# Kernel optimization log

Hardware: AMD Instinct MI355X
Metric: run time of the kernel (lower is better)

The kernel has to match this reference:

```python
import jax, jax.numpy as jnp
import numpy as np

DIM, HEADS, DIM_HEAD = 512, 8, 64

def setup_inputs() -> dict:
    key = jax.random.key(0)
    ks = jax.random.split(key, 9)
    B, T = 4, 4096
    s = 1.0 / np.sqrt(DIM)
    x = jax.random.normal(ks[0], (B, T, DIM), dtype=jnp.float32)
    Wq = jax.random.uniform(ks[1], (DIM, DIM), jnp.float32, -s, s)
    Wk = jax.random.uniform(ks[2], (DIM, DIM), jnp.float32, -s, s)
    Wv = jax.random.uniform(ks[3], (DIM, DIM), jnp.float32, -s, s)
    Wp = jax.random.uniform(ks[4], (DIM, DIM), jnp.float32, -s, s)
    bq = jax.random.uniform(ks[5], (DIM,), jnp.float32, -s, s)
    bk = jax.random.uniform(ks[6], (DIM,), jnp.float32, -s, s)
    bv = jax.random.uniform(ks[7], (DIM,), jnp.float32, -s, s)
    bp = jax.random.uniform(ks[8], (DIM,), jnp.float32, -s, s)
    return {"x": x, "Wq": Wq, "bq": bq, "Wk": Wk, "bk": bk,
            "Wv": Wv, "bv": bv, "Wp": Wp, "bp": bp}

def reference(x, Wq, bq, Wk, bk, Wv, bv, Wp, bp):
    B, T, _ = x.shape
    H, D = HEADS, DIM_HEAD
    # projections -> [B, H, T, D]
    def proj(W, b):
        return (x @ W.T + b).reshape(B, T, H, D).transpose(0, 2, 1, 3)
    q = jax.nn.softmax(proj(Wq, bq), axis=-1)
    k = jax.nn.softmax(proj(Wk, bk), axis=-1)
    v = proj(Wv, bv)
    # l1 normalization: D_inv = 1 / <q, sum_t k>
    k_sum = k.sum(axis=2, keepdims=True)                 # [B,H,1,D]
    D_inv = 1.0 / (q * k_sum).sum(axis=-1, keepdims=True)  # [B,H,T,1]
    context = jnp.einsum('bhtd,bhte->bhde', k, v)        # small DxD per head
    out = jnp.einsum('bhtd,bhde->bhte', q, context) * D_inv + q
    out = out.transpose(0, 2, 1, 3).reshape(B, T, H * D)
    return out @ Wp.T + bp
```

## Files before the change

kernel.cpp:

```cpp
#include <hip/hip_runtime.h>

#define NTOK  16384
#define KDIM  512
#define NQKV  1536
#define TT    4096

using frag8   = __attribute__((ext_vector_type(8))) short;
using floatx4 = __attribute__((ext_vector_type(4))) float;

__device__ __forceinline__ unsigned short f2b(float f) {
  union { float f; unsigned u; } v; v.f = f;
  unsigned r = v.u + 0x7fffu + ((v.u >> 16) & 1u);
  return (unsigned short)(r >> 16);
}
__device__ __forceinline__ float b2f(unsigned short s) {
  union { unsigned u; float f; } v; v.u = ((unsigned)s) << 16; return v.f;
}
__device__ __forceinline__ float blo(unsigned w) {
  union { unsigned u; float f; } v; v.u = w << 16; return v.f;
}
__device__ __forceinline__ float bhi(unsigned w) {
  union { unsigned u; float f; } v; v.u = w & 0xffff0000u; return v.f;
}

__device__ __forceinline__ void gl_lds16(const void* g, void* l) {
  __builtin_amdgcn_global_load_lds((__attribute__((address_space(1))) const void*)g,
                                   (__attribute__((address_space(3))) void*)l,
                                   16, 0, 0);
}

__global__ __launch_bounds__(256) void cvt_all(
    const float* __restrict__ x,
    const float* __restrict__ Wq, const float* __restrict__ Wk,
    const float* __restrict__ Wv, const float* __restrict__ Wp,
    const float* __restrict__ bq, const float* __restrict__ bk,
    const float* __restrict__ bv,
    unsigned short* __restrict__ xb,
    unsigned short* __restrict__ wqkv, unsigned short* __restrict__ wp,
    float* __restrict__ bias_qkv) {
  const int blk = blockIdx.x;
  if (blk < 8192) {
    const size_t i = (size_t)blk * 256 + threadIdx.x;
    const float4 v = ((const float4*)x)[i];
    ushort4 o;
    o.x = f2b(v.x); o.y = f2b(v.y); o.z = f2b(v.z); o.w = f2b(v.w);
    ((ushort4*)xb)[i] = o;
    return;
  }
  const int idx = (blk - 8192) * 256 + threadIdx.x;
  if (idx < 786432) {
    const int m = idx >> 9, i = idx & 511;
    const float* W = (m < 512) ? Wq : ((m < 1024) ? Wk : Wv);
    wqkv[idx] = f2b(W[(m & 511) * 512 + i]);
    return;
  }
  const int j = idx - 786432;
  if (j < 262144) { wp[j] = f2b(Wp[j]); return; }
  const int c = j - 262144;
  if (c < 1536)
    bias_qkv[c] = (c < 512) ? bq[c] : ((c < 1024) ? bk[c - 512] : bv[c - 1024]);
}

template<int SOFT>
__global__ __launch_bounds__(256, 2) void gemm_bt(
    const unsigned short* __restrict__ A,
    const unsigned short* __restrict__ Bm,
    const float* __restrict__ bias,
    void* __restrict__ C,
    int M, int N, int K, int ldc)
{
  __shared__ unsigned short sh[32768];
  const int tid  = threadIdx.x;
  const int wave = tid >> 6;
  const int lane = tid & 63;
  const int quad = lane >> 4;
  const int lr   = lane & 15;
  const int sw7  = lr & 7;
  const int bid  = ((blockIdx.x & 7) * (gridDim.x >> 3)) + (blockIdx.x >> 3);
  const int nt   = N >> 7;
  const int bn   = (bid % nt) << 7;
  const int bm   = (bid / nt) << 7;
  const int half = wave >> 1;
  const int wm   = half << 6;
  const int wn   = (wave & 1) << 6;

  floatx4 acc[4][4] = {};

  const int srow = tid >> 3;
  const int scol = ((tid & 7) ^ ((tid >> 3) & 7)) << 3;
  const unsigned short* Ag = A + (size_t)(bm + srow) * K + scol;
  const unsigned short* Bg = Bm + (size_t)(bn + srow) * K + scol;

  auto STAGE = [&](unsigned short* base, int k0) {
    unsigned short* Al = base + (wave << 9);
    unsigned short* Bl = Al + 8192;
    gl_lds16(Ag + k0,                    Al);
    gl_lds16(Ag + (size_t)32 * K + k0,   Al + 2048);
    gl_lds16(Ag + (size_t)64 * K + k0,   Al + 4096);
    gl_lds16(Ag + (size_t)96 * K + k0,   Al + 6144);
    gl_lds16(Bg + k0,                    Bl);
    gl_lds16(Bg + (size_t)32 * K + k0,   Bl + 2048);
    gl_lds16(Bg + (size_t)64 * K + k0,   Bl + 4096);
    gl_lds16(Bg + (size_t)96 * K + k0,   Bl + 6144);
  };

  auto COMPUTE = [&](const unsigned short* Asb) {
    const unsigned short* Bsb = Asb + 8192;
#pragma unroll
    for (int kk = 0; kk < 2; kk++) {
      const int coff = ((((kk << 2) + quad) ^ sw7) << 3);
      frag8 af[4], bf[4];
#pragma unroll
      for (int i = 0; i < 4; i++)
        af[i] = *(const frag8*)&Asb[(wm + (i << 4) + lr) * 64 + coff];
#pragma unroll
      for (int j = 0; j < 4; j++)
        bf[j] = *(const frag8*)&Bsb[(wn + (j << 4) + lr) * 64 + coff];
#pragma unroll
      for (int i = 0; i < 4; i++)
#pragma unroll
        for (int j = 0; j < 4; j++)
          acc[i][j] = __builtin_amdgcn_mfma_f32_16x16x32_bf16(af[i], bf[j], acc[i][j], 0, 0, 0);
    }
  };

  STAGE(sh, 0);
  __syncthreads();

  for (int k0 = 0; k0 < K; k0 += 128) {
    STAGE(sh + 16384, k0 + 64);
    COMPUTE(sh);
    __syncthreads();
    if (k0 + 128 < K) STAGE(sh, k0 + 128);
    COMPUTE(sh + 16384);
    __syncthreads();
  }

  const int ccol0 = bn + wn + lr;

#pragma unroll
  for (int j = 0; j < 4; j++) {
    const float bv = bias[ccol0 + (j << 4)];
#pragma unroll
    for (int i = 0; i < 4; i++)
#pragma unroll
      for (int r = 0; r < 4; r++)
        acc[i][j][r] += bv;
  }

  if (SOFT) {
    const int region = (bn + wn) >> 9;
    if (region < 2) {
#pragma unroll
      for (int i = 0; i < 4; i++)
#pragma unroll
        for (int r = 0; r < 4; r++) {
          float e0 = __expf(acc[i][0][r]);
          float e1 = __expf(acc[i][1][r]);
          float e2 = __expf(acc[i][2][r]);
          float e3 = __expf(acc[i][3][r]);
          float s = e0 + e1 + e2 + e3;
          s += __shfl_xor(s, 1);
          s += __shfl_xor(s, 2);
          s += __shfl_xor(s, 4);
          s += __shfl_xor(s, 8);
          const float inv = 1.f / s;
          acc[i][0][r] = e0 * inv; acc[i][1][r] = e1 * inv;
          acc[i][2][r] = e2 * inv; acc[i][3][r] = e3 * inv;
        }
    }
    unsigned short* os = sh;
#pragma unroll
    for (int p = 0; p < 2; p++) {
      __syncthreads();
      if (half == p) {
#pragma unroll
        for (int i = 0; i < 4; i++)
#pragma unroll
          for (int j = 0; j < 4; j++)
#pragma unroll
            for (int r = 0; r < 4; r++)
              os[((i << 4) + (quad << 2) + r) * 132 + wn + (j << 4) + lr] = f2b(acc[i][j][r]);
      }
      __syncthreads();
#pragma unroll
      for (int it = 0; it < 4; it++) {
        const int idx = (it << 8) + tid;
        const int row = idx >> 4;
        const int c8  = (idx & 15) << 3;
        *(uint4*)((unsigned short*)C + (size_t)(bm + (p << 6) + row) * ldc + bn + c8) =
            *(const uint4*)&os[row * 132 + c8];
      }
    }
  } else {
    float* osf = (float*)sh;
#pragma unroll
    for (int p = 0; p < 2; p++) {
      __syncthreads();
      if (half == p) {
#pragma unroll
        for (int i = 0; i < 4; i++)
#pragma unroll
          for (int j = 0; j < 4; j++)
#pragma unroll
            for (int r = 0; r < 4; r++)
              osf[((i << 4) + (quad << 2) + r) * 130 + wn + (j << 4) + lr] = acc[i][j][r];
      }
      __syncthreads();
#pragma unroll
      for (int it = 0; it < 8; it++) {
        const int idx = (it << 8) + tid;
        const int row = idx >> 5;
        const int c4  = (idx & 31) << 2;
        *(float4*)((float*)C + (size_t)(bm + (p << 6) + row) * ldc + bn + c4) =
            *(const float4*)&osf[row * 130 + c4];
      }
    }
  }
}

__global__ __launch_bounds__(256) void kv_context(const unsigned short* __restrict__ qkv,
                                                  float* __restrict__ part,
                                                  float* __restrict__ ksp) {
  const int bid = blockIdx.x;
  const int tc  = bid & 15;
  const int bh  = bid >> 4;
  const int b   = bh >> 3, h = bh & 7;
  __shared__ float ks[16 * 64];
  __shared__ float vs[16 * 64];
  const int tid = threadIdx.x;
  const int ty = tid >> 4, tx = tid & 15;
  floatx4 acc[4] = {};
  floatx4 ksacc = {0.f, 0.f, 0.f, 0.f};

  const int si    = tid << 3;
  const int strow = si >> 7;
  const int sw    = si & 127;
  const int t0    = b * TT + tc * 256;
  const unsigned short* gcol = qkv + ((sw < 64) ? (512 + h * 64 + sw)
                                                : (1024 + h * 64 + (sw - 64)));
  float* sdst = (sw < 64) ? &ks[strow * 64 + sw] : &vs[strow * 64 + (sw - 64)];

  uint4 raw = *(const uint4*)(gcol + (size_t)(t0 + strow) * NQKV);
  for (int tt = 0; tt < 256; tt += 16) {
    __syncthreads();
    const floatx4 f0 = {blo(raw.x), bhi(raw.x), blo(raw.y), bhi(raw.y)};
    const floatx4 f1 = {blo(raw.z), bhi(raw.z), blo(raw.w), bhi(raw.w)};
    *(floatx4*)sdst = f0;
    *(floatx4*)(sdst + 4) = f1;
    __syncthreads();
    if (tt + 16 < 256)
      raw = *(const uint4*)(gcol + (size_t)(t0 + tt + 16 + strow) * NQKV);
#pragma unroll
    for (int t = 0; t < 16; t++) {
      const floatx4 vb = *(const floatx4*)&vs[t * 64 + (ty << 2)];
      const floatx4 kb = *(const floatx4*)&ks[t * 64 + (tx << 2)];
      acc[0] += vb.x * kb;
      acc[1] += vb.y * kb;
      acc[2] += vb.z * kb;
      acc[3] += vb.w * kb;
    }
    ksacc += *(const floatx4*)&ks[ty * 64 + (tx << 2)];
  }
  __syncthreads();
  *(floatx4*)&vs[ty * 64 + (tx << 2)] = ksacc;
  __syncthreads();

  float* pg = part + ((size_t)(tc * 32 + bh) << 12) + (size_t)(ty << 2) * 64 + (tx << 2);
#pragma unroll
  for (int i = 0; i < 4; i++)
    *(floatx4*)(pg + i * 64) = acc[i];

  if (tid < 64) {
    float s = 0.f;
    for (int t2 = 0; t2 < 16; t2++) s += vs[t2 * 64 + tid];
    ksp[(tc * 32 + bh) * 64 + tid] = s;
  }
}

__global__ __launch_bounds__(256) void ctx_reduce(const float* __restrict__ part,
                                                  const float* __restrict__ ksp,
                                                  unsigned short* __restrict__ ctxb) {
  const int bh = blockIdx.x / 5, g = blockIdx.x % 5;
  const int row = (g << 4) + (threadIdx.x >> 4);
  const int d0  = (threadIdx.x & 15) << 2;
  floatx4 s = {0.f, 0.f, 0.f, 0.f};
  if (row < 64) {
    const float* p = part + ((size_t)bh << 12) + row * 64 + d0;
    for (int c = 0; c < 16; c++)
      s += *(const floatx4*)(p + ((size_t)c << 17));
  } else if (row == 64) {
    const float* p = ksp + bh * 64 + d0;
    for (int c = 0; c < 16; c++)
      s += *(const floatx4*)(p + (c << 11));
  }
  ushort4 o;
  o.x = f2b(s.x); o.y = f2b(s.y); o.z = f2b(s.z); o.w = f2b(s.w);
  *(ushort4*)&ctxb[(size_t)bh * 5120 + (row << 6) + d0] = o;
}

__global__ __launch_bounds__(256) void attn_out(const unsigned short* __restrict__ qkv,
                                                const unsigned short* __restrict__ ctxb,
                                                unsigned short* __restrict__ opre) {
  const int tc = blockIdx.x >> 5;
  const int bh = blockIdx.x & 31;
  const int b = bh >> 3, h = bh & 7;
  const int t0 = b * TT + (tc << 6);
  __shared__ unsigned short sh[144 * 72];
  unsigned short* qs = sh;
  unsigned short* cs = sh + 64 * 72;
  unsigned short* os = cs;
  const int tid = threadIdx.x;

  for (int i = tid; i < 512; i += 256) {
    const int row = i >> 3, c8 = (i & 7) << 3;
    *(uint4*)&qs[row * 72 + c8] =
        *(const uint4*)&qkv[(size_t)(t0 + row) * NQKV + h * 64 + c8];
  }
  for (int i = tid; i < 640; i += 256) {
    const int row = i >> 3, c8 = (i & 7) << 3;
    *(uint4*)&cs[row * 72 + c8] =
        *(const uint4*)&ctxb[(size_t)bh * 5120 + (row << 6) + c8];
  }
  __syncthreads();

  const int lane = tid & 63, w = tid >> 6, quad = lane >> 4, lr = lane & 15;
  floatx4 acc[5] = {};
#pragma unroll
  for (int k2 = 0; k2 < 2; k2++) {
    const int d0 = (k2 << 5) + (quad << 3);
    const frag8 bf = *(const frag8*)&qs[((w << 4) + lr) * 72 + d0];
#pragma unroll
    for (int et = 0; et < 5; et++) {
      const frag8 af = *(const frag8*)&cs[(et * 16 + lr) * 72 + d0];
      acc[et] = __builtin_amdgcn_mfma_f32_16x16x32_bf16(af, bf, acc[et], 0, 0, 0);
    }
  }
  const float dinv = 1.f / __shfl(acc[4][0], lr);
  __syncthreads();

  const int trow = (w << 4) + lr;
#pragma unroll
  for (int et = 0; et < 4; et++)
#pragma unroll
    for (int r = 0; r < 4; r++) {
      const int e = et * 16 + (quad << 2) + r;
      const float qv = b2f(qs[trow * 72 + e]);
      os[trow * 72 + e] = f2b(acc[et][r] * dinv + qv);
    }
  __syncthreads();

  for (int i = tid; i < 512; i += 256) {
    const int row = i >> 3, c8 = (i & 7) << 3;
    *(uint4*)&opre[(size_t)(t0 + row) * KDIM + h * 64 + c8] = *(const uint4*)&os[row * 72 + c8];
  }
}

extern "C" void kernel_launch(void* const* d_in, const int* in_sizes, int n_in,
                              void* d_out, int out_size, void* d_ws, size_t ws_size,
                              hipStream_t stream) {
  (void)in_sizes; (void)n_in; (void)out_size; (void)ws_size;
  const float* x  = (const float*)d_in[0];
  const float* Wq = (const float*)d_in[1];
  const float* bq = (const float*)d_in[2];
  const float* Wk = (const float*)d_in[3];
  const float* bk = (const float*)d_in[4];
  const float* Wv = (const float*)d_in[5];
  const float* bv = (const float*)d_in[6];
  const float* Wp = (const float*)d_in[7];
  const float* bp = (const float*)d_in[8];

  char* w = (char*)d_ws;
  unsigned short* xb   = (unsigned short*)w; w += (size_t)NTOK * KDIM * 2;
  float* part          = (float*)xb;
  unsigned short* wqkv = (unsigned short*)w; w += (size_t)NQKV * KDIM * 2;
  unsigned short* wp   = (unsigned short*)w; w += (size_t)KDIM * KDIM * 2;
  float* bias_qkv      = (float*)w;          w += (size_t)NQKV * 4;
  float* ksp           = (float*)w;          w += (size_t)1024 * 64 * 4;
  unsigned short* ctxb = (unsigned short*)w; w += (size_t)32 * 80 * 64 * 2;
  unsigned short* qkv  = (unsigned short*)w; w += (size_t)NTOK * NQKV * 2;
  unsigned short* opre = (unsigned short*)w; w += (size_t)NTOK * KDIM * 2;

  cvt_all<<<12294, 256, 0, stream>>>(x, Wq, Wk, Wv, Wp, bq, bk, bv,
                                     xb, wqkv, wp, bias_qkv);
  gemm_bt<1><<<(NTOK / 128) * (NQKV / 128), 256, 0, stream>>>(
      xb, wqkv, bias_qkv, qkv, NTOK, NQKV, KDIM, NQKV);
  kv_context<<<512, 256, 0, stream>>>(qkv, part, ksp);
  ctx_reduce<<<160, 256, 0, stream>>>(part, ksp, ctxb);
  attn_out<<<2048, 256, 0, stream>>>(qkv, ctxb, opre);
  gemm_bt<0><<<(NTOK / 128) * (KDIM / 128), 256, 0, stream>>>(
      opre, wp, bp, d_out, NTOK, KDIM, KDIM, KDIM);
}
```

Measured before the change: 186.7 us.

## Enlarge GEMM tiles to 256x256 with 8-wave blocks and phased MFMA pipeline

Both GEMMs now use 512-thread blocks. The QKV projection uses 256x256 tiles and the output projection uses 128x256 tiles, with double-buffered direct-to-LDS loads and manual vmcnt/lgkmcnt waits and raw barriers. The inner loop is split into four phases that interleave LDS fragment reads with MFMA bursts at raised wave priority, and issues the next prefetch mid-iteration. This raises arithmetic intensity and reduces global traffic per FLOP, but it uses more LDS and registers, and fewer blocks (384/256) may underfill the CUs.

```diff
diff --git a/kernel.cpp b/kernel.cpp
--- a/kernel.cpp
+++ b/kernel.cpp
@@ -8,6 +8,12 @@
 using frag8   = __attribute__((ext_vector_type(8))) short;
 using floatx4 = __attribute__((ext_vector_type(4))) float;
 
+#define SBAR()    asm volatile("s_barrier" ::: "memory")
+#define WAITLG()  do { asm volatile("s_waitcnt lgkmcnt(0)" ::: "memory"); \
+                       __builtin_amdgcn_sched_barrier(0); } while (0)
+#define WAITVM(N) do { asm volatile("s_waitcnt vmcnt(" #N ")" ::: "memory"); \
+                       __builtin_amdgcn_sched_barrier(0); } while (0)
+
 __device__ __forceinline__ unsigned short f2b(float f) {
   union { float f; unsigned u; } v; v.f = f;
   unsigned r = v.u + 0x7fffu + ((v.u >> 16) & 1u);
@@ -27,6 +33,9 @@
   __builtin_amdgcn_global_load_lds((__attribute__((address_space(1))) const void*)g,
                                    (__attribute__((address_space(3))) void*)l,
                                    16, 0, 0);
+}
+__device__ __forceinline__ floatx4 mfma16(frag8 a, frag8 b, floatx4 c) {
+  return __builtin_amdgcn_mfma_f32_16x16x32_bf16(a, b, c, 0, 0, 0);
 }
 
 __global__ __launch_bounds__(256) void cvt_all(
@@ -61,100 +70,157 @@
     bias_qkv[c] = (c < 512) ? bq[c] : ((c < 1024) ? bk[c - 512] : bv[c - 1024]);
 }
 
-template<int SOFT>
-__global__ __launch_bounds__(256, 2) void gemm_bt(
+template<int SOFT, int IQ>
+__global__ __launch_bounds__(512, 2) void gemm_bt(
     const unsigned short* __restrict__ A,
     const unsigned short* __restrict__ Bm,
     const float* __restrict__ bias,
     void* __restrict__ C,
     int M, int N, int K, int ldc)
 {
-  __shared__ unsigned short sh[32768];
+  constexpr int BUFS = IQ * 4096 + 16384;
+  __shared__ unsigned short sh[2 * BUFS];
   const int tid  = threadIdx.x;
   const int wave = tid >> 6;
   const int lane = tid & 63;
   const int quad = lane >> 4;
   const int lr   = lane & 15;
-  const int sw7  = lr & 7;
+  const int wr   = wave >> 2;
+  const int wc   = wave & 3;
   const int bid  = ((blockIdx.x & 7) * (gridDim.x >> 3)) + (blockIdx.x >> 3);
-  const int nt   = N >> 7;
-  const int bn   = (bid % nt) << 7;
-  const int bm   = (bid / nt) << 7;
-  const int half = wave >> 1;
-  const int wm   = half << 6;
-  const int wn   = (wave & 1) << 6;
-
-  floatx4 acc[4][4] = {};
-
-  const int srow = tid >> 3;
-  const int scol = ((tid & 7) ^ ((tid >> 3) & 7)) << 3;
-  const unsigned short* Ag = A + (size_t)(bm + srow) * K + scol;
-  const unsigned short* Bg = Bm + (size_t)(bn + srow) * K + scol;
-
-  auto STAGE = [&](unsigned short* base, int k0) {
-    unsigned short* Al = base + (wave << 9);
-    unsigned short* Bl = Al + 8192;
-    gl_lds16(Ag + k0,                    Al);
-    gl_lds16(Ag + (size_t)32 * K + k0,   Al + 2048);
-    gl_lds16(Ag + (size_t)64 * K + k0,   Al + 4096);
-    gl_lds16(Ag + (size_t)96 * K + k0,   Al + 6144);
-    gl_lds16(Bg + k0,                    Bl);
-    gl_lds16(Bg + (size_t)32 * K + k0,   Bl + 2048);
-    gl_lds16(Bg + (size_t)64 * K + k0,   Bl + 4096);
-    gl_lds16(Bg + (size_t)96 * K + k0,   Bl + 6144);
+  const int nt   = N >> 8;
+  const int bn   = (bid % nt) << 8;
+  const int bm   = (bid / nt) * (IQ << 6);
+
+  floatx4 acc[2 * IQ][4] = {};
+
+  const int l8  = lane >> 3;
+  const int csw = ((lane & 7) ^ l8) << 3;
+  const unsigned short* Ast = A + (size_t)(bm + (wave << 3) + l8) * K + csw;
+  const unsigned short* Bst = Bm + (size_t)(bn + (wave << 3) + l8) * K + csw;
+  unsigned short* const st0 = sh + (wave << 9);
+
+  auto STAGE = [&](int bsel, int kc) {
+    unsigned short* base = st0 + bsel * BUFS;
+#pragma unroll
+    for (int r2 = 0; r2 < IQ; ++r2)
+      gl_lds16(Ast + (size_t)(r2 << 6) * K + kc, base + (r2 << 12));
+#pragma unroll
+    for (int r2 = 0; r2 < 4; ++r2)
+      gl_lds16(Bst + (size_t)(r2 << 6) * K + kc, base + (IQ << 12) + (r2 << 12));
   };
 
-  auto COMPUTE = [&](const unsigned short* Asb) {
-    const unsigned short* Bsb = Asb + 8192;
-#pragma unroll
-    for (int kk = 0; kk < 2; kk++) {
-      const int coff = ((((kk << 2) + quad) ^ sw7) << 3);
-      frag8 af[4], bf[4];
-#pragma unroll
-      for (int i = 0; i < 4; i++)
-        af[i] = *(const frag8*)&Asb[(wm + (i << 4) + lr) * 64 + coff];
-#pragma unroll
-      for (int j = 0; j < 4; j++)
-        bf[j] = *(const frag8*)&Bsb[(wn + (j << 4) + lr) * 64 + coff];
-#pragma unroll
-      for (int i = 0; i < 4; i++)
-#pragma unroll
-        for (int j = 0; j < 4; j++)
-          acc[i][j] = __builtin_amdgcn_mfma_f32_16x16x32_bf16(af[i], bf[j], acc[i][j], 0, 0, 0);
-    }
-  };
-
-  STAGE(sh, 0);
-  __syncthreads();
-
-  for (int k0 = 0; k0 < K; k0 += 128) {
-    STAGE(sh + 16384, k0 + 64);
-    COMPUTE(sh);
-    __syncthreads();
-    if (k0 + 128 < K) STAGE(sh, k0 + 128);
-    COMPUTE(sh + 16384);
-    __syncthreads();
-  }
-
-  const int ccol0 = bn + wn + lr;
-
-#pragma unroll
-  for (int j = 0; j < 4; j++) {
+  const int arow  = ((wr * (IQ << 5)) + lr) << 6;
+  const int brow  = ((wc << 6) + lr) << 6;
+  const int k0off = ((quad ^ (lr & 7)) << 3);
+  const int k1off = (((4 + quad) ^ (lr & 7)) << 3);
+
+  STAGE(0, 0);
+  STAGE(1, 64);
+  if constexpr (IQ == 4) WAITVM(8); else WAITVM(6);
+  SBAR();
+
+  const int NT = K >> 6;
+  for (int t = 0; t < NT; ++t) {
+    const int b = t & 1;
+    const unsigned short* Ab = sh + b * BUFS;
+    const unsigned short* Bb = Ab + (IQ << 12);
+
+    frag8 av[IQ][2], b1[2][2], b2[2][2];
+
+#pragma unroll
+    for (int i = 0; i < IQ; ++i) {
+      av[i][0] = *(const frag8*)&Ab[arow + (i << 10) + k0off];
+      av[i][1] = *(const frag8*)&Ab[arow + (i << 10) + k1off];
+    }
+#pragma unroll
+    for (int j = 0; j < 2; ++j) {
+      b1[j][0] = *(const frag8*)&Bb[brow + (j << 10) + k0off];
+      b1[j][1] = *(const frag8*)&Bb[brow + (j << 10) + k1off];
+    }
+    SBAR(); WAITLG();
+    __builtin_amdgcn_s_setprio(1);
+#pragma unroll
+    for (int i = 0; i < IQ; ++i)
+#pragma unroll
+      for (int j = 0; j < 2; ++j) {
+        acc[i][j] = mfma16(av[i][0], b1[j][0], acc[i][j]);
+        acc[i][j] = mfma16(av[i][1], b1[j][1], acc[i][j]);
+      }
+    __builtin_amdgcn_s_setprio(0);
+    SBAR();
+
+#pragma unroll
+    for (int j = 0; j < 2; ++j) {
+      b2[j][0] = *(const frag8*)&Bb[brow + ((j + 2) << 10) + k0off];
+      b2[j][1] = *(const frag8*)&Bb[brow + ((j + 2) << 10) + k1off];
+    }
+    SBAR(); WAITLG();
+    __builtin_amdgcn_s_setprio(1);
+#pragma unroll
+    for (int i = 0; i < IQ; ++i)
+#pragma unroll
+      for (int j = 0; j < 2; ++j) {
+        acc[i][j + 2] = mfma16(av[i][0], b2[j][0], acc[i][j + 2]);
+        acc[i][j + 2] = mfma16(av[i][1], b2[j][1], acc[i][j + 2]);
+      }
+    __builtin_amdgcn_s_setprio(0);
+    SBAR();
+
+#pragma unroll
+    for (int i = 0; i < IQ; ++i) {
+      av[i][0] = *(const frag8*)&Ab[arow + ((i + IQ) << 10) + k0off];
+      av[i][1] = *(const frag8*)&Ab[arow + ((i + IQ) << 10) + k1off];
+    }
+    SBAR(); WAITLG();
+    __builtin_amdgcn_s_setprio(1);
+#pragma unroll
+    for (int i = 0; i < IQ; ++i)
+#pragma unroll
+      for (int j = 0; j < 2; ++j) {
+        acc[i + IQ][j] = mfma16(av[i][0], b1[j][0], acc[i + IQ][j]);
+        acc[i + IQ][j] = mfma16(av[i][1], b1[j][1], acc[i + IQ][j]);
+      }
+    __builtin_amdgcn_s_setprio(0);
+    SBAR();
+
+    if (t + 2 < NT) STAGE(b, (t + 2) << 6);
+    SBAR();
+    __builtin_amdgcn_s_setprio(1);
+#pragma unroll
+    for (int i = 0; i < IQ; ++i)
+#pragma unroll
+      for (int j = 0; j < 2; ++j) {
+        acc[i + IQ][j + 2] = mfma16(av[i][0], b2[j][0], acc[i + IQ][j + 2]);
+        acc[i + IQ][j + 2] = mfma16(av[i][1], b2[j][1], acc[i + IQ][j + 2]);
+      }
+    __builtin_amdgcn_s_setprio(0);
+    if (t + 2 < NT) {
+      if constexpr (IQ == 4) WAITVM(8); else WAITVM(6);
+    } else if (t + 2 == NT) {
+      WAITVM(0);
+    }
+    SBAR();
+  }
+
+  const int ccol0 = bn + (wc << 6) + lr;
+#pragma unroll
+  for (int j = 0; j < 4; ++j) {
     const float bv = bias[ccol0 + (j << 4)];
 #pragma unroll
-    for (int i = 0; i < 4; i++)
-#pragma unroll
-      for (int r = 0; r < 4; r++)
+    for (int i = 0; i < 2 * IQ; ++i)
+#pragma unroll
+      for (int r = 0; r < 4; ++r)
         acc[i][j][r] += bv;
   }
 
   if (SOFT) {
-    const int region = (bn + wn) >> 9;
+    const int region = (bn + (wc << 6)) >> 9;
     if (region < 2) {
 #pragma unroll
-      for (int i = 0; i < 4; i++)
-#pragma unroll
-        for (int r = 0; r < 4; r++) {
+      for (int i = 0; i < 2 * IQ; ++i)
+#pragma unroll
+        for (int r = 0; r < 4; ++r) {
           float e0 = __expf(acc[i][0][r]);
           float e1 = __expf(acc[i][1][r]);
           float e2 = __expf(acc[i][2][r]);
@@ -171,49 +237,52 @@
     }
     unsigned short* os = sh;
 #pragma unroll
-    for (int p = 0; p < 2; p++) {
+    for (int p = 0; p < 2; ++p) {
       __syncthreads();
-      if (half == p) {
-#pragma unroll
-        for (int i = 0; i < 4; i++)
-#pragma unroll
-          for (int j = 0; j < 4; j++)
-#pragma unroll
-            for (int r = 0; r < 4; r++)
-              os[((i << 4) + (quad << 2) + r) * 132 + wn + (j << 4) + lr] = f2b(acc[i][j][r]);
+      if (wr == p) {
+#pragma unroll
+        for (int i = 0; i < 2 * IQ; ++i)
+#pragma unroll
+          for (int j = 0; j < 4; ++j)
+#pragma unroll
+            for (int r = 0; r < 4; ++r)
+              os[((i << 4) + (quad << 2) + r) * 272 + (wc << 6) + (j << 4) + lr] =
+                  f2b(acc[i][j][r]);
       }
       __syncthreads();
 #pragma unroll
-      for (int it = 0; it < 4; it++) {
-        const int idx = (it << 8) + tid;
-        const int row = idx >> 4;
-        const int c8  = (idx & 15) << 3;
-        *(uint4*)((unsigned short*)C + (size_t)(bm + (p << 6) + row) * ldc + bn + c8) =
-            *(const uint4*)&os[row * 132 + c8];
+      for (int it = 0; it < 2 * IQ; ++it) {
+        const int idx = (it << 9) + tid;
+        const int row = idx >> 5;
+        const int c8  = (idx & 31) << 3;
+        *(uint4*)((unsigned short*)C + (size_t)(bm + p * (IQ << 5) + row) * ldc + bn + c8) =
+            *(const uint4*)&os[row * 272 + c8];
       }
     }
   } else {
     float* osf = (float*)sh;
 #pragma unroll
-    for (int p = 0; p < 2; p++) {
+    for (int p = 0; p < IQ; ++p) {
       __syncthreads();
-      if (half == p) {
-#pragma unroll
-        for (int i = 0; i < 4; i++)
-#pragma unroll
-          for (int j = 0; j < 4; j++)
-#pragma unroll
-            for (int r = 0; r < 4; r++)
-              osf[((i << 4) + (quad << 2) + r) * 130 + wn + (j << 4) + lr] = acc[i][j][r];
+      if (wr == (IQ == 4 ? (p >> 1) : p)) {
+        const int fb = (IQ == 4 ? (p & 1) << 2 : 0);
+#pragma unroll
+        for (int i2 = 0; i2 < 4; ++i2)
+#pragma unroll
+          for (int j = 0; j < 4; ++j)
+#pragma unroll
+            for (int r = 0; r < 4; ++r)
+              osf[((i2 << 4) + (quad << 2) + r) * 260 + (wc << 6) + (j << 4) + lr] =
+                  acc[fb + i2][j][r];
       }
       __syncthreads();
 #pragma unroll
-      for (int it = 0; it < 8; it++) {
-        const int idx = (it << 8) + tid;
-        const int row = idx >> 5;
-        const int c4  = (idx & 31) << 2;
+      for (int it = 0; it < 8; ++it) {
+        const int idx = (it << 9) + tid;
+        const int row = idx >> 6;
+        const int c4  = (idx & 63) << 2;
         *(float4*)((float*)C + (size_t)(bm + (p << 6) + row) * ldc + bn + c4) =
-            *(const float4*)&osf[row * 130 + c4];
+            *(const float4*)&osf[row * 260 + c4];
       }
     }
   }
@@ -383,11 +452,11 @@
 
   cvt_all<<<12294, 256, 0, stream>>>(x, Wq, Wk, Wv, Wp, bq, bk, bv,
                                      xb, wqkv, wp, bias_qkv);
-  gemm_bt<1><<<(NTOK / 128) * (NQKV / 128), 256, 0, stream>>>(
+  gemm_bt<1, 4><<<384, 512, 0, stream>>>(
       xb, wqkv, bias_qkv, qkv, NTOK, NQKV, KDIM, NQKV);
   kv_context<<<512, 256, 0, stream>>>(qkv, part, ksp);
   ctx_reduce<<<160, 256, 0, stream>>>(part, ksp, ctxb);
   attn_out<<<2048, 256, 0, stream>>>(qkv, ctxb, opre);
-  gemm_bt<0><<<(NTOK / 128) * (KDIM / 128), 256, 0, stream>>>(
+  gemm_bt<0, 2><<<256, 512, 0, stream>>>(
       opre, wp, bp, d_out, NTOK, KDIM, KDIM, KDIM);
 }
```

New measurement: 195.3 us. 1.05x slower.
